# Optimization experiments

Hardware: AMD Instinct MI355X
Metric: run time of the kernel (lower is better)

## Reference

```python
import jax, jax.numpy as jnp
import numpy as np

NUM_KEYPOINTS = 2048
SAMPLE_RADIUS = 1.6
NUM_SECTORS = 6
NEG = jnp.float32(-1e10)
POS = jnp.float32(1e10)


def setup_inputs() -> dict:
    key = jax.random.key(0)
    kxy, kz, kc, kcz, kd, ky = jax.random.split(key, 6)
    B, N, M = 2, 65536, 128
    pts_xy = jax.random.uniform(kxy, (B, N, 2), minval=-70.0, maxval=70.0)
    pts_z = jax.random.uniform(kz, (B, N, 1), minval=-3.0, maxval=1.0)
    points = jnp.concatenate([pts_xy, pts_z], axis=-1)  # [B,N,3]
    ctr_xy = jax.random.uniform(kc, (B, M, 2), minval=-60.0, maxval=60.0)
    ctr_z = jax.random.uniform(kcz, (B, M, 1), minval=-2.0, maxval=0.0)
    dims = jax.random.uniform(kd, (B, M, 3), minval=1.0, maxval=4.5)
    yaw = jax.random.uniform(ky, (B, M, 1), minval=-np.pi, maxval=np.pi)
    rois = jnp.concatenate([ctr_xy, ctr_z, dims, yaw], axis=-1)  # [B,M,7]
    return {"points": points, "rois": rois}


def _masked_fps(xyz, mask, K):
    """Farthest point sampling restricted to mask; returns K indices into xyz.
    Matches mmcv furthest_point_sample: squared distances, start at first point."""
    first = jnp.argmax(mask)  # first valid point in original order
    dmin = jnp.where(mask, POS, NEG)

    def step(carry, _):
        dmin, last = carry
        d = jnp.sum((xyz - xyz[last]) ** 2, axis=-1)
        dmin = jnp.minimum(dmin, jnp.where(mask, d, NEG))
        nxt = jnp.argmax(dmin)
        return (dmin, nxt), nxt

    (_, _), rest = jax.lax.scan(step, (dmin, first), None, length=K - 1)
    return jnp.concatenate([first[None], rest])  # [K]


def _spc_single(points, rois):
    """points: [N,3] float, rois: [M,7]. Returns [NUM_KEYPOINTS,3]."""
    N = points.shape[0]
    K = NUM_KEYPOINTS
    # geometric center: z += dz/2 (done in forward before sampling)
    rois = rois.at[:, 2].add(rois[:, 5] * 0.5)
    # --- sample_points_with_roi: point-to-ROI-center distance filter ---
    diff = points[:, None, :] - rois[None, :, 0:3]          # [N,M,3]
    dist = jnp.linalg.norm(diff, axis=-1)                   # [N,M]
    min_dis = jnp.min(dist, axis=-1)
    min_idx = jnp.argmin(dist, axis=-1)
    roi_max_dim = jnp.linalg.norm(rois[min_idx, 3:6] * 0.5, axis=-1)
    valid = min_dis < roi_max_dim + SAMPLE_RADIUS           # [N]
    total = jnp.maximum(jnp.sum(valid), 1)
    # --- sector_fps ---
    sector_size = 2.0 * np.pi / NUM_SECTORS
    angles = jnp.arctan2(points[:, 1], points[:, 0]) + np.pi
    sector = jnp.clip(jnp.floor(angles / sector_size), 0, NUM_SECTORS).astype(jnp.int32)
    masks = valid[None, :] & (sector[None, :] == jnp.arange(NUM_SECTORS)[:, None])  # [S,N]
    cnt = jnp.sum(masks, axis=-1)                           # [S]
    # per-sector budget: min(cnt_k, ceil(cnt_k / total * K)), 0 for empty sectors
    n_k = jnp.minimum(cnt, jnp.ceil(cnt.astype(jnp.float32) * K / total).astype(cnt.dtype))
    fps_idx = jax.vmap(_masked_fps, in_axes=(None, 0, None))(points, masks, K)  # [S,K]
    # concatenate the first n_k picks of each sector in sector order
    offsets = jnp.concatenate([jnp.zeros((1,), n_k.dtype), jnp.cumsum(n_k)[:-1]])
    pos = offsets[:, None] + jnp.arange(K)[None, :]          # [S,K] slot in concat order
    keep = jnp.arange(K)[None, :] < n_k[:, None]
    pos = jnp.where(keep, pos, K)                            # out-of-range -> dropped
    buf = jnp.zeros((K,), jnp.int32)
    buf = buf.at[pos.reshape(-1)].set(fps_idx.reshape(-1).astype(jnp.int32), mode='drop')
    # truncate / cyclic-repeat to exactly K keypoints
    s_total = jnp.maximum(jnp.sum(n_k), 1)
    out_idx = buf[jnp.arange(K) % s_total]
    return points[out_idx]                                   # [K,3]


def reference(points, rois):
    return jax.vmap(_spc_single)(points, rois)  # [B,K,3]
```

## Files before the change

kernel.cpp:

```cpp
#include <hip/hip_runtime.h>
#include <cmath>
#include <cstdint>

#pragma clang fp contract(off)

#define B_ 2
#define N_ 65536
#define M_ 128
#define K_ 2048
#define S_ 6
#define NBLK 256
#define CT 256
#define FPS_T 256
#define NW 4
#define RMAX 16
#define CAP (FPS_T * RMAX)

#define PI_F 3.14159265358979323846f
#define SS_F 1.0471975511965976f

__device__ __forceinline__ unsigned long long wave_max_u64_dpp(unsigned long long key) {
#define DPP_STEP(CTRL)                                                          \
    {                                                                           \
        unsigned lo = (unsigned)key, hi = (unsigned)(key >> 32);                \
        unsigned olo = (unsigned)__builtin_amdgcn_update_dpp(0, (int)lo, CTRL, 0xf, 0xf, true); \
        unsigned ohi = (unsigned)__builtin_amdgcn_update_dpp(0, (int)hi, CTRL, 0xf, 0xf, true); \
        unsigned long long o = ((unsigned long long)ohi << 32) | olo;           \
        if (o > key) key = o;                                                   \
    }
    DPP_STEP(0x111)
    DPP_STEP(0x112)
    DPP_STEP(0x114)
    DPP_STEP(0x118)
    DPP_STEP(0x142)
    DPP_STEP(0x143)
#undef DPP_STEP
    return key;
}

__global__ __launch_bounds__(CT)
void k_classify(const float* __restrict__ points, const float* __restrict__ rois,
                int* __restrict__ sec_id, int* __restrict__ blkcnt) {
    __shared__ float4 sroi[M_];
    __shared__ int lc[8];
    int blk = blockIdx.x;
    int gid = blk * CT + threadIdx.x;
    int b = gid >> 16;
    if (threadIdx.x < M_) {
        const float* r = rois + ((size_t)b * M_ + threadIdx.x) * 7;
        float cz = r[2] + r[5] * 0.5f;
        float hx = r[3] * 0.5f, hy = r[4] * 0.5f, hz = r[5] * 0.5f;
        sroi[threadIdx.x] = make_float4(r[0], r[1], cz, sqrtf((hx*hx + hy*hy) + hz*hz));
    }
    if (threadIdx.x < 8) lc[threadIdx.x] = 0;
    __syncthreads();

    const float* p = points + (size_t)gid * 3;
    float px = p[0], py = p[1], pz = p[2];
    float best = 1e30f; int bi = 0;
    for (int m = 0; m < M_; m++) {
        float4 c = sroi[m];
        float dx = px - c.x, dy = py - c.y, dz = pz - c.z;
        float d = sqrtf((dx*dx + dy*dy) + dz*dz);
        if (d < best) { best = d; bi = m; }
    }
    bool valid = best < (sroi[bi].w + 1.6f);

    float a = atan2f(py, px) + PI_F;
    float fs = floorf(a / SS_F);
    fs = fminf(fmaxf(fs, 0.0f), 6.0f);
    int sec = (int)fs;

    sec_id[gid] = valid ? sec : -1;
    if (valid) atomicAdd(&lc[sec], 1);
    __syncthreads();
    if (threadIdx.x < 8) blkcnt[blk * 8 + threadIdx.x] = lc[threadIdx.x];
}

__global__ void k_plan(const int* __restrict__ blkcnt, int* __restrict__ bbase,
                       int* __restrict__ cnt, int* __restrict__ offv,
                       int* __restrict__ n_needed, int* __restrict__ sec_base,
                       int* __restrict__ s_total) {
    __shared__ int scnt[2][8];
    int t = threadIdx.x;
    if (t < 16) scnt[t >> 3][t & 7] = 0;
    __syncthreads();
    if (t < 14) {
        int b = t / 7, s = t % 7;
        int run = 0;
        for (int j = 0; j < NBLK; j++) {
            int blk = b * NBLK + j;
            int c = blkcnt[blk * 8 + s];
            if (s < 6) bbase[blk * 6 + s] = run;
            run += c;
        }
        scnt[b][s] = run;
        cnt[b * 8 + s] = run;
    }
    __syncthreads();
    if (t < B_) {
        int b = t;
        int total = 0;
        for (int s = 0; s < 7; s++) total += scnt[b][s];
        if (total < 1) total = 1;
        int sb = 0, snk = 0;
        for (int s = 0; s < 6; s++) {
            int cs = scnt[b][s];
            int nk = (int)ceilf((float)cs * 2048.0f / (float)total);
            if (nk > cs) nk = cs;
            offv[b * 6 + s] = snk;
            int need = 0;
            if (snk < K_) { need = K_ - snk; if (need > nk) need = nk; }
            n_needed[b * 6 + s] = need;
            sec_base[b * 6 + s] = sb;
            sb += cs; snk += nk;
        }
        s_total[b] = (snk < 1) ? 1 : snk;
    }
}

__global__ __launch_bounds__(CT)
void k_compact(const float* __restrict__ points, const int* __restrict__ sec_id,
               const int* __restrict__ sec_base, const int* __restrict__ bbase,
               int* __restrict__ comp_idx, float4* __restrict__ comp_xyz) {
    __shared__ int lc[4 * 6];
    __shared__ int sbase[6], blkb[6];
    int blk = blockIdx.x;
    int b = blk >> 8;
    int tid = threadIdx.x, lane = tid & 63, wid = tid >> 6;
    if (tid < 6) sbase[tid] = sec_base[b * 6 + tid];
    else if (tid >= 64 && tid < 70) blkb[tid - 64] = bbase[blk * 6 + (tid - 64)];
    int gid = blk * CT + tid;
    int sec = sec_id[gid];
    unsigned long long mymask = 0;
    for (int s = 0; s < 6; s++) {
        unsigned long long m = __ballot(sec == s);
        if (sec == s) mymask = m;
        if (lane == 0) lc[wid * 6 + s] = __popcll(m);
    }
    __syncthreads();
    if (sec >= 0 && sec < 6) {
        int woff = 0;
        for (int w = 0; w < wid; w++) woff += lc[w * 6 + sec];
        int rank = __popcll(mymask & ((1ull << lane) - 1ull));
        int addr = b * N_ + sbase[sec] + blkb[sec] + woff + rank;
        const float* p = points + (size_t)gid * 3;
        comp_idx[addr] = gid & (N_ - 1);
        comp_xyz[addr] = make_float4(p[0], p[1], p[2], 0.0f);
    }
}

__global__ __launch_bounds__(FPS_T, 3)
void k_fps(const int* __restrict__ cnt, const int* __restrict__ sec_base,
           const int* __restrict__ offv, const int* __restrict__ n_needed,
           const float4* __restrict__ comp_xyz,
           float* __restrict__ dmin_g, int* __restrict__ buf) {
    __shared__ float4 sxyz[CAP];
    __shared__ int pick_lds[K_];
    __shared__ unsigned long long skey[2][NW];
    int b = blockIdx.x / S_, s = blockIdx.x % S_;
    int need = n_needed[b * 6 + s];
    if (need <= 0) return;
    int cs = cnt[b * 8 + s];
    int base = b * N_ + sec_base[b * 6 + s];
    const float4* cxyz = comp_xyz + base;
    int off = b * K_ + offv[b * 6 + s];
    int tid = threadIdx.x, lane = tid & 63, wid = tid >> 6;

    if (cs <= CAP) {
        float px[RMAX], py[RMAX], pz[RMAX], dmv[RMAX];
        #pragma unroll
        for (int r = 0; r < RMAX; r++) {
            if (r * FPS_T < cs) {
                int i = tid + r * FPS_T;
                if (i < cs) {
                    float4 q = cxyz[i];
                    sxyz[i] = q;
                    px[r] = q.x; py[r] = q.y; pz[r] = q.z;
                    dmv[r] = 1e10f;
                }
            }
        }
        if (tid == 0) pick_lds[0] = 0;
        __syncthreads();
        float4 l4 = sxyz[0];
        float lx = l4.x, ly = l4.y, lz = l4.z;

        #pragma unroll 1
        for (int k = 1; k < need; k++) {
            unsigned long long key = 0;
            #pragma unroll
            for (int r = 0; r < RMAX; r++) {
                if (r * FPS_T < cs) {
                    int i = tid + r * FPS_T;
                    if (i < cs) {
                        float dx = px[r] - lx, dy = py[r] - ly, dz = pz[r] - lz;
                        float d = (dx*dx + dy*dy) + dz*dz;
                        float nd = fminf(dmv[r], d);
                        dmv[r] = nd;
                        unsigned long long kk =
                            ((unsigned long long)__float_as_uint(nd) << 32) | (unsigned)(~(unsigned)i);
                        if (kk > key) key = kk;
                    }
                }
            }
            key = wave_max_u64_dpp(key);
            int par = k & 1;
            if (lane == 63) skey[par][wid] = key;
            __syncthreads();
            unsigned long long bk = skey[par][0];
            if (skey[par][1] > bk) bk = skey[par][1];
            if (skey[par][2] > bk) bk = skey[par][2];
            if (skey[par][3] > bk) bk = skey[par][3];
            int bix = (int)(~(unsigned)(bk & 0xFFFFFFFFull));
            if (tid == 0) pick_lds[k] = bix;
            float4 n4 = sxyz[bix];
            lx = n4.x; ly = n4.y; lz = n4.z;
        }
        __syncthreads();
        #pragma unroll 1
        for (int i = tid; i < need; i += FPS_T)
            buf[off + i] = base + pick_lds[i];
    } else {
        float* dm = dmin_g + base;
        if (tid == 0) pick_lds[0] = 0;
        __syncthreads();
        float4 f0 = cxyz[0];
        float lx = f0.x, ly = f0.y, lz = f0.z;
        #pragma unroll 1
        for (int k = 1; k < need; k++) {
            unsigned long long key = 0;
            #pragma unroll 1
            for (int i = tid; i < cs; i += FPS_T) {
                float4 q = cxyz[i];
                float dx = q.x - lx, dy = q.y - ly, dz = q.z - lz;
                float d = (dx*dx + dy*dy) + dz*dz;
                float prev = (k == 1) ? 1e10f : dm[i];
                float nd = fminf(prev, d);
                dm[i] = nd;
                unsigned long long kk =
                    ((unsigned long long)__float_as_uint(nd) << 32) | (unsigned)(~(unsigned)i);
                if (kk > key) key = kk;
            }
            key = wave_max_u64_dpp(key);
            int par = k & 1;
            if (lane == 63) skey[par][wid] = key;
            __syncthreads();
            unsigned long long bk = skey[par][0];
            if (skey[par][1] > bk) bk = skey[par][1];
            if (skey[par][2] > bk) bk = skey[par][2];
            if (skey[par][3] > bk) bk = skey[par][3];
            int bix = (int)(~(unsigned)(bk & 0xFFFFFFFFull));
            if (tid == 0) pick_lds[k] = bix;
            float4 n4 = cxyz[bix];
            lx = n4.x; ly = n4.y; lz = n4.z;
        }
        __syncthreads();
        #pragma unroll 1
        for (int i = tid; i < need; i += FPS_T)
            buf[off + i] = base + pick_lds[i];
    }
}

__global__ void k_out(const float* __restrict__ points, const int* __restrict__ buf,
                      const int* __restrict__ comp_idx, const int* __restrict__ s_total,
                      float* __restrict__ out) {
    int i = blockIdx.x * 256 + threadIdx.x;
    if (i >= B_ * K_) return;
    int b = i / K_, j = i % K_;
    int st = s_total[b];
    int g = buf[b * K_ + (j % st)];
    int idx = comp_idx[g];
    const float* p = points + ((size_t)b * N_ + idx) * 3;
    float* o = out + (size_t)i * 3;
    o[0] = p[0]; o[1] = p[1]; o[2] = p[2];
}

extern "C" void kernel_launch(void* const* d_in, const int* in_sizes, int n_in,
                              void* d_out, int out_size, void* d_ws, size_t ws_size,
                              hipStream_t stream) {
    const float* points = (const float*)d_in[0];
    const float* rois   = (const float*)d_in[1];
    float* out = (float*)d_out;

    char* w = (char*)d_ws;
    auto carve = [&](size_t bytes) -> char* {
        char* p = w; w += (bytes + 255) & ~(size_t)255; return p;
    };
    int*    sec_id   = (int*)   carve((size_t)B_ * N_ * sizeof(int));
    int*    blkcnt   = (int*)   carve((size_t)B_ * NBLK * 8 * sizeof(int));
    int*    bbase    = (int*)   carve((size_t)B_ * NBLK * 6 * sizeof(int));
    int*    cnt      = (int*)   carve((size_t)B_ * 8 * sizeof(int));
    int*    offv     = (int*)   carve((size_t)B_ * 6 * sizeof(int));
    int*    n_needed = (int*)   carve((size_t)B_ * 6 * sizeof(int));
    int*    sec_base = (int*)   carve((size_t)B_ * 6 * sizeof(int));
    int*    s_total  = (int*)   carve((size_t)B_ * sizeof(int));
    int*    buf      = (int*)   carve((size_t)B_ * K_ * sizeof(int));
    int*    comp_idx = (int*)   carve((size_t)B_ * N_ * sizeof(int));
    float4* comp_xyz = (float4*)carve((size_t)B_ * N_ * sizeof(float4));
    float*  dmin_g   = (float*) carve((size_t)B_ * N_ * sizeof(float));

    hipLaunchKernelGGL(k_classify, dim3(B_ * NBLK), dim3(CT), 0, stream,
                       points, rois, sec_id, blkcnt);
    hipLaunchKernelGGL(k_plan, dim3(1), dim3(64), 0, stream,
                       blkcnt, bbase, cnt, offv, n_needed, sec_base, s_total);
    hipLaunchKernelGGL(k_compact, dim3(B_ * NBLK), dim3(CT), 0, stream,
                       points, sec_id, sec_base, bbase, comp_idx, comp_xyz);
    hipLaunchKernelGGL(k_fps, dim3(B_ * S_), dim3(FPS_T), 0, stream,
                       cnt, sec_base, offv, n_needed, comp_xyz, dmin_g, buf);
    hipLaunchKernelGGL(k_out, dim3((B_ * K_ + 255) / 256), dim3(256), 0, stream,
                       points, buf, comp_idx, s_total, out);
}
```

Measured before the change: 473.6 us.

## Run small-sector FPS on a single wavefront without block barriers

For sectors with at most 2048 candidate points, FPS now runs on one 64-lane wavefront. Each lane holds up to 32 points in registers, and the per-iteration argmax uses a float max reduction followed by a min-index reduction, both through DPP and readlane. This removes the per-step __syncthreads and LDS key exchange that dominate the serial 2048-step loop, and picks are written straight to global memory. In exchange, each wave does up to 8x more ALU work per step, register pressure rises (launch bounds go from 3 to 2 blocks), and correctness relies on the first-index tie-break still matching the reference.

```diff
diff --git a/kernel.cpp b/kernel.cpp
--- a/kernel.cpp
+++ b/kernel.cpp
@@ -15,10 +15,33 @@
 #define NW 4
 #define RMAX 16
 #define CAP (FPS_T * RMAX)
+#define WCAP 2048
 
 #define PI_F 3.14159265358979323846f
 #define SS_F 1.0471975511965976f
 
+__device__ __forceinline__ float wave_max_f32_dpp(float v) {
+#define STEP(CTRL)                                                              \
+    {                                                                           \
+        int o = __builtin_amdgcn_update_dpp(__float_as_int(v), __float_as_int(v), \
+                                            CTRL, 0xf, 0xf, false);             \
+        v = fmaxf(v, __int_as_float(o));                                        \
+    }
+    STEP(0x111) STEP(0x112) STEP(0x114) STEP(0x118) STEP(0x142) STEP(0x143)
+#undef STEP
+    return v;
+}
+__device__ __forceinline__ unsigned wave_min_u32_dpp(unsigned v) {
+#define STEP(CTRL)                                                              \
+    {                                                                           \
+        unsigned o = (unsigned)__builtin_amdgcn_update_dpp((int)v, (int)v,      \
+                                            CTRL, 0xf, 0xf, false);             \
+        v = (o < v) ? o : v;                                                    \
+    }
+    STEP(0x111) STEP(0x112) STEP(0x114) STEP(0x118) STEP(0x142) STEP(0x143)
+#undef STEP
+    return v;
+}
 __device__ __forceinline__ unsigned long long wave_max_u64_dpp(unsigned long long key) {
 #define DPP_STEP(CTRL)                                                          \
     {                                                                           \
@@ -28,15 +51,17 @@
         unsigned long long o = ((unsigned long long)ohi << 32) | olo;           \
         if (o > key) key = o;                                                   \
     }
-    DPP_STEP(0x111)
-    DPP_STEP(0x112)
-    DPP_STEP(0x114)
-    DPP_STEP(0x118)
-    DPP_STEP(0x142)
-    DPP_STEP(0x143)
+    DPP_STEP(0x111) DPP_STEP(0x112) DPP_STEP(0x114)
+    DPP_STEP(0x118) DPP_STEP(0x142) DPP_STEP(0x143)
 #undef DPP_STEP
     return key;
 }
+
+struct FpsShared {
+    float4 sxyz[CAP];
+    int    pick[K_];
+    alignas(16) unsigned long long skey[2][NW];
+};
 
 __global__ __launch_bounds__(CT)
 void k_classify(const float* __restrict__ points, const float* __restrict__ rois,
@@ -88,6 +113,7 @@
     if (t < 14) {
         int b = t / 7, s = t % 7;
         int run = 0;
+        #pragma unroll 8
         for (int j = 0; j < NBLK; j++) {
             int blk = b * NBLK + j;
             int c = blkcnt[blk * 8 + s];
@@ -150,14 +176,58 @@
     }
 }
 
-__global__ __launch_bounds__(FPS_T, 3)
+template<int R>
+__device__ __forceinline__
+void fps_wave(const float4* __restrict__ cxyz, float4* __restrict__ sxyz,
+              int cs, int need, int base, int off, int* __restrict__ buf,
+              int lane) {
+    float px[R], py[R], pz[R], dmv[R];
+    #pragma unroll
+    for (int r = 0; r < R; r++) {
+        int i = r * 64 + lane;
+        if (i < cs) {
+            float4 q = cxyz[i];
+            sxyz[i] = q;
+            px[r] = q.x; py[r] = q.y; pz[r] = q.z;
+            dmv[r] = 1e10f;
+        } else {
+            px[r] = 0.0f; py[r] = 0.0f; pz[r] = 0.0f;
+            dmv[r] = -1e30f;
+        }
+    }
+    if (lane == 0) buf[off] = base;
+    if (need == 1) return;
+    float4 f0 = cxyz[0];
+    float lx = f0.x, ly = f0.y, lz = f0.z;
+
+    #pragma unroll 1
+    for (int k = 1; k < need; k++) {
+        float bv = -1.0f; int bi = 0;
+        #pragma unroll
+        for (int r = 0; r < R; r++) {
+            float dx = px[r] - lx, dy = py[r] - ly, dz = pz[r] - lz;
+            float d = (dx*dx + dy*dy) + dz*dz;
+            float nd = fminf(dmv[r], d);
+            dmv[r] = nd;
+            if (nd > bv) { bv = nd; bi = r * 64 + lane; }
+        }
+        float mv = wave_max_f32_dpp(bv);
+        float maxv = __int_as_float(__builtin_amdgcn_readlane(__float_as_int(mv), 63));
+        unsigned idx = (bv == maxv) ? (unsigned)bi : 0xFFFFFFFFu;
+        idx = wave_min_u32_dpp(idx);
+        int wi = (int)(unsigned)__builtin_amdgcn_readlane((int)idx, 63);
+        if (lane == 0) buf[off + k] = base + wi;
+        float4 n4 = sxyz[wi];
+        lx = n4.x; ly = n4.y; lz = n4.z;
+    }
+}
+
+__global__ __launch_bounds__(FPS_T, 2)
 void k_fps(const int* __restrict__ cnt, const int* __restrict__ sec_base,
            const int* __restrict__ offv, const int* __restrict__ n_needed,
            const float4* __restrict__ comp_xyz,
            float* __restrict__ dmin_g, int* __restrict__ buf) {
-    __shared__ float4 sxyz[CAP];
-    __shared__ int pick_lds[K_];
-    __shared__ unsigned long long skey[2][NW];
+    __shared__ FpsShared sh;
     int b = blockIdx.x / S_, s = blockIdx.x % S_;
     int need = n_needed[b * 6 + s];
     if (need <= 0) return;
@@ -167,23 +237,30 @@
     int off = b * K_ + offv[b * 6 + s];
     int tid = threadIdx.x, lane = tid & 63, wid = tid >> 6;
 
+    if (cs <= WCAP) {
+        if (wid != 0) return;
+        if      (cs <=  512) fps_wave< 8>(cxyz, sh.sxyz, cs, need, base, off, buf, lane);
+        else if (cs <= 1024) fps_wave<16>(cxyz, sh.sxyz, cs, need, base, off, buf, lane);
+        else if (cs <= 1536) fps_wave<24>(cxyz, sh.sxyz, cs, need, base, off, buf, lane);
+        else                 fps_wave<32>(cxyz, sh.sxyz, cs, need, base, off, buf, lane);
+        return;
+    }
+
     if (cs <= CAP) {
         float px[RMAX], py[RMAX], pz[RMAX], dmv[RMAX];
         #pragma unroll
         for (int r = 0; r < RMAX; r++) {
-            if (r * FPS_T < cs) {
-                int i = tid + r * FPS_T;
-                if (i < cs) {
-                    float4 q = cxyz[i];
-                    sxyz[i] = q;
-                    px[r] = q.x; py[r] = q.y; pz[r] = q.z;
-                    dmv[r] = 1e10f;
-                }
+            int i = tid + r * FPS_T;
+            if (i < cs) {
+                float4 q = cxyz[i];
+                sh.sxyz[i] = q;
+                px[r] = q.x; py[r] = q.y; pz[r] = q.z;
+                dmv[r] = 1e10f;
             }
         }
-        if (tid == 0) pick_lds[0] = 0;
+        if (tid == 0) sh.pick[0] = 0;
         __syncthreads();
-        float4 l4 = sxyz[0];
+        float4 l4 = sh.sxyz[0];
         float lx = l4.x, ly = l4.y, lz = l4.z;
 
         #pragma unroll 1
@@ -191,39 +268,37 @@
             unsigned long long key = 0;
             #pragma unroll
             for (int r = 0; r < RMAX; r++) {
-                if (r * FPS_T < cs) {
-                    int i = tid + r * FPS_T;
-                    if (i < cs) {
-                        float dx = px[r] - lx, dy = py[r] - ly, dz = pz[r] - lz;
-                        float d = (dx*dx + dy*dy) + dz*dz;
-                        float nd = fminf(dmv[r], d);
-                        dmv[r] = nd;
-                        unsigned long long kk =
-                            ((unsigned long long)__float_as_uint(nd) << 32) | (unsigned)(~(unsigned)i);
-                        if (kk > key) key = kk;
-                    }
+                int i = tid + r * FPS_T;
+                if (i < cs) {
+                    float dx = px[r] - lx, dy = py[r] - ly, dz = pz[r] - lz;
+                    float d = (dx*dx + dy*dy) + dz*dz;
+                    float nd = fminf(dmv[r], d);
+                    dmv[r] = nd;
+                    unsigned long long kk =
+                        ((unsigned long long)__float_as_uint(nd) << 32) | (unsigned)(~(unsigned)i);
+                    if (kk > key) key = kk;
                 }
             }
             key = wave_max_u64_dpp(key);
             int par = k & 1;
-            if (lane == 63) skey[par][wid] = key;
+            if (lane == 63) sh.skey[par][wid] = key;
             __syncthreads();
-            unsigned long long bk = skey[par][0];
-            if (skey[par][1] > bk) bk = skey[par][1];
-            if (skey[par][2] > bk) bk = skey[par][2];
-            if (skey[par][3] > bk) bk = skey[par][3];
+            unsigned long long bk = sh.skey[par][0];
+            if (sh.skey[par][1] > bk) bk = sh.skey[par][1];
+            if (sh.skey[par][2] > bk) bk = sh.skey[par][2];
+            if (sh.skey[par][3] > bk) bk = sh.skey[par][3];
             int bix = (int)(~(unsigned)(bk & 0xFFFFFFFFull));
-            if (tid == 0) pick_lds[k] = bix;
-            float4 n4 = sxyz[bix];
+            if (tid == 0) sh.pick[k] = bix;
+            float4 n4 = sh.sxyz[bix];
             lx = n4.x; ly = n4.y; lz = n4.z;
         }
         __syncthreads();
         #pragma unroll 1
         for (int i = tid; i < need; i += FPS_T)
-            buf[off + i] = base + pick_lds[i];
+            buf[off + i] = base + sh.pick[i];
     } else {
         float* dm = dmin_g + base;
-        if (tid == 0) pick_lds[0] = 0;
+        if (tid == 0) sh.pick[0] = 0;
         __syncthreads();
         float4 f0 = cxyz[0];
         float lx = f0.x, ly = f0.y, lz = f0.z;
@@ -244,21 +319,21 @@
             }
             key = wave_max_u64_dpp(key);
             int par = k & 1;
-            if (lane == 63) skey[par][wid] = key;
+            if (lane == 63) sh.skey[par][wid] = key;
             __syncthreads();
-            unsigned long long bk = skey[par][0];
-            if (skey[par][1] > bk) bk = skey[par][1];
-            if (skey[par][2] > bk) bk = skey[par][2];
-            if (skey[par][3] > bk) bk = skey[par][3];
+            unsigned long long bk = sh.skey[par][0];
+            if (sh.skey[par][1] > bk) bk = sh.skey[par][1];
+            if (sh.skey[par][2] > bk) bk = sh.skey[par][2];
+            if (sh.skey[par][3] > bk) bk = sh.skey[par][3];
             int bix = (int)(~(unsigned)(bk & 0xFFFFFFFFull));
-            if (tid == 0) pick_lds[k] = bix;
+            if (tid == 0) sh.pick[k] = bix;
             float4 n4 = cxyz[bix];
             lx = n4.x; ly = n4.y; lz = n4.z;
         }
         __syncthreads();
         #pragma unroll 1
         for (int i = tid; i < need; i += FPS_T)
-            buf[off + i] = base + pick_lds[i];
+            buf[off + i] = base + sh.pick[i];
     }
 }
 
```

Measured after the change: 569.6 us. 20.3% more time.
